# Kernel tuning notes

Hardware: AMD Instinct MI355X
Metric: run time of the kernel (lower is better)

Reference implementation:

```python
import jax, jax.numpy as jnp
import numpy as np

NUM_GRAPHS = 64
NUM_EDGE_TYPES = 3


def gat_conv(x, src, dst, W, a_src, a_dst, bias, num_nodes, heads, ch):
    # PyG GATConv, concat=False: mean over heads, attention leaky_relu slope 0.2
    xp = (x @ W).reshape(num_nodes, heads, ch)          # [N,H,C]
    al_s = jnp.einsum('nhc,hc->nh', xp, a_src)           # [N,H]
    al_d = jnp.einsum('nhc,hc->nh', xp, a_dst)
    logits = jax.nn.leaky_relu(al_s[src] + al_d[dst], 0.2)  # [E,H]
    m = jax.ops.segment_max(logits, dst, num_segments=num_nodes)
    e = jnp.exp(logits - m[dst])
    denom = jax.ops.segment_sum(e, dst, num_segments=num_nodes)
    alpha = e / denom[dst]                               # segment softmax over dst
    msg = alpha[:, :, None] * xp[src]                    # [E,H,C]
    out = jax.ops.segment_sum(msg, dst, num_segments=num_nodes)  # [N,H,C]
    return out.mean(axis=1) + bias


def lstm_dir(seq, w_ih, w_hh, b_ih, b_hh):
    # seq: [L,N,C]; PyTorch LSTM cell math
    hh = w_hh.shape[1]
    n = seq.shape[1]
    def step(carry, xt):
        h, c = carry
        g = xt @ w_ih.T + b_ih + h @ w_hh.T + b_hh
        i, f, gg, o = jnp.split(g, 4, axis=-1)
        c = jax.nn.sigmoid(f) * c + jax.nn.sigmoid(i) * jnp.tanh(gg)
        h = jax.nn.sigmoid(o) * jnp.tanh(c)
        return (h, c), h
    init = (jnp.zeros((n, hh), seq.dtype), jnp.zeros((n, hh), seq.dtype))
    _, hs = jax.lax.scan(step, init, seq)
    return hs  # [L,N,hh]


def setup_inputs() -> dict:
    key = jax.random.key(0)
    ks = jax.random.split(key, 24)
    N, E, C, H, P, T = 50000, 600000, 128, 4, 2, NUM_EDGE_TYPES
    HH = (P * C) // 2  # JK biLSTM hidden = 128
    s = 0.05
    src = jax.random.randint(ks[0], (E,), 0, N, dtype=jnp.int32)
    off = jax.random.randint(ks[1], (E,), 1, N, dtype=jnp.int32)
    dst = (src + off) % N  # guaranteed self-loop free
    edge_index = jnp.stack([src, dst], axis=0)  # types are contiguous blocks of E//T
    batch = jnp.sort(jax.random.randint(ks[2], (N,), 0, NUM_GRAPHS, dtype=jnp.int32))
    return {
        'x': jax.random.normal(ks[3], (N, C), jnp.float32),
        'edge_index': edge_index,
        'batch': batch,
        'problem_type': jax.random.uniform(ks[4], (NUM_GRAPHS, 1), jnp.float32),
        'gat_W': jax.random.normal(ks[5], (P, T, C, H * C), jnp.float32) * s,
        'gat_att_src': jax.random.normal(ks[6], (P, T, H, C), jnp.float32) * s,
        'gat_att_dst': jax.random.normal(ks[7], (P, T, H, C), jnp.float32) * s,
        'gat_bias': jnp.zeros((P, T, C), jnp.float32),
        'w_ih_fw': jax.random.normal(ks[8], (4 * HH, C), jnp.float32) * s,
        'w_hh_fw': jax.random.normal(ks[9], (4 * HH, HH), jnp.float32) * s,
        'b_ih_fw': jnp.zeros((4 * HH,), jnp.float32),
        'b_hh_fw': jnp.zeros((4 * HH,), jnp.float32),
        'w_ih_bw': jax.random.normal(ks[10], (4 * HH, C), jnp.float32) * s,
        'w_hh_bw': jax.random.normal(ks[11], (4 * HH, HH), jnp.float32) * s,
        'b_ih_bw': jnp.zeros((4 * HH,), jnp.float32),
        'b_hh_bw': jnp.zeros((4 * HH,), jnp.float32),
        'jk_att_w': jax.random.normal(ks[12], (2 * HH, 1), jnp.float32) * s,
        'jk_att_b': jnp.zeros((1,), jnp.float32),
        'fc1_w': jax.random.normal(ks[13], (C + 1, 80), jnp.float32) * s,
        'fc1_b': jnp.zeros((80,), jnp.float32),
        'fc2_w': jax.random.normal(ks[14], (80, 80), jnp.float32) * s,
        'fc2_b': jnp.zeros((80,), jnp.float32),
        'fc3_w': jax.random.normal(ks[15], (80, 10), jnp.float32) * s,
        'fc3_b': jnp.zeros((10,), jnp.float32),
    }


def reference(x, edge_index, batch, problem_type, gat_W, gat_att_src, gat_att_dst,
              gat_bias, w_ih_fw, w_hh_fw, b_ih_fw, b_hh_fw, w_ih_bw, w_hh_bw,
              b_ih_bw, b_hh_bw, jk_att_w, jk_att_b, fc1_w, fc1_b, fc2_w, fc2_b,
              fc3_w, fc3_b):
    N, C = x.shape
    P, T, H, _ = gat_att_src.shape
    E = edge_index.shape[1]
    Et = E // T  # edge types stored in contiguous blocks
    loop = jnp.arange(N, dtype=edge_index.dtype)
    xs = [x]
    cur = x
    for p in range(P):
        acc = jnp.zeros_like(cur)
        for t in range(T):
            src = jnp.concatenate([edge_index[0, t * Et:(t + 1) * Et], loop])
            dst = jnp.concatenate([edge_index[1, t * Et:(t + 1) * Et], loop])
            out = gat_conv(cur, src, dst, gat_W[p, t], gat_att_src[p, t],
                           gat_att_dst[p, t], gat_bias[p, t], N, H, C)
            acc = acc + jax.nn.leaky_relu(out)  # slope 0.01 (F.leaky_relu default)
        cur = acc / T
        xs.append(cur)
    seq = jnp.stack(xs, axis=0)  # [L,N,C], L=P+1
    hf = lstm_dir(seq, w_ih_fw, w_hh_fw, b_ih_fw, b_hh_fw)
    hb = lstm_dir(seq[::-1], w_ih_bw, w_hh_bw, b_ih_bw, b_hh_bw)[::-1]
    h = jnp.concatenate([hf, hb], axis=-1)  # [L,N,2*HH]
    score = jnp.einsum('lnh,ho->lno', h, jk_att_w)[..., 0] + jk_att_b[0]  # [L,N]
    alpha = jax.nn.softmax(score, axis=0)
    xjk = jnp.einsum('ln,lnc->nc', alpha, seq)  # JK-LSTM weighted sum
    pooled = jax.ops.segment_sum(xjk, batch, num_segments=NUM_GRAPHS)  # collate='sum'
    z = jnp.concatenate([pooled, problem_type], axis=1)
    z = jax.nn.leaky_relu(z @ fc1_w + fc1_b)
    z = jax.nn.leaky_relu(z @ fc2_w + fc2_b)
    return z @ fc3_w + fc3_b
```

## Files before the change

### kernel.cpp

```cpp
#include <hip/hip_runtime.h>
#include <cfloat>


typedef __attribute__((ext_vector_type(8))) short short8;
typedef __attribute__((ext_vector_type(4))) float f32x4;

#define DEG_CAP 31

__device__ __forceinline__ float lrelu(float x, float s) { return x > 0.f ? x : s * x; }

__device__ __forceinline__ float sigmf(float x) {
    return __builtin_amdgcn_rcpf(1.f + __expf(-x));
}
__device__ __forceinline__ float tanhf_fast(float x) {
    x = fminf(fmaxf(x, -15.f), 15.f);
    float e = __expf(2.f * x);
    return (e - 1.f) * __builtin_amdgcn_rcpf(e + 1.f);
}

__device__ __forceinline__ unsigned f2bf(float f) {
    unsigned u = __float_as_uint(f);
    return (u + 0x7FFFu + ((u >> 16) & 1u)) >> 16;
}
__device__ __forceinline__ float bf2f(ushort u) {
    return __uint_as_float(((unsigned)u) << 16);
}
__device__ __forceinline__ float bflo(unsigned u) {
    return __uint_as_float(u << 16);
}
__device__ __forceinline__ float bfhi(unsigned u) {
    return __uint_as_float(u & 0xFFFF0000u);
}

__device__ __forceinline__ int xcd_tile(int bid, int nwg) {
    int q = nwg >> 3, r = nwg & 7;
    int xcd = bid & 7, idx = bid >> 3;
    return (xcd < r ? xcd * (q + 1) : r * (q + 1) + (xcd - r) * q) + idx;
}

__device__ __forceinline__ void stage_a16(
    char* ldsA, const ushort* __restrict__ A, int row0, int M, int tid)
{
#pragma unroll
    for (int it = 0; it < 4; ++it) {
        int idx = it * 512 + tid;
        int r = idx >> 4, kc = (idx & 15) << 3;
        int row = row0 + r;
        uint4 v = make_uint4(0, 0, 0, 0);
        if (row < M) v = *(const uint4*)(A + (long)row * 128 + kc);
        *(uint4*)(ldsA + ((r * 256 + kc * 2) ^ ((r & 7) << 4))) = v;
    }
}
__device__ __forceinline__ void stage_b16(
    char* ldsB, const ushort* __restrict__ B, int tid)
{
#pragma unroll
    for (int it = 0; it < 4; ++it) {
        int idx = it * 512 + tid;
        int r = idx >> 4, kc = (idx & 15) << 3;
        *(uint4*)(ldsB + ((r * 256 + kc * 2) ^ ((r & 7) << 4))) =
            *(const uint4*)(B + (long)r * 128 + kc);
    }
}

__device__ __forceinline__ void compute_tile(
    const char* ldsA, const char* ldsB, f32x4 acc[2][4],
    int wr, int wc, int lr, int lk)
{
#pragma unroll
    for (int ks = 0; ks < 4; ++ks) {
        int kb = ks * 64 + lk;
        short8 af[2], bfr[4];
#pragma unroll
        for (int i = 0; i < 2; ++i) {
            int r = wr + i * 16 + lr;
            af[i] = *(const short8*)(ldsA + ((r * 256 + kb) ^ ((r & 7) << 4)));
        }
#pragma unroll
        for (int j = 0; j < 4; ++j) {
            int c = wc + j * 16 + lr;
            bfr[j] = *(const short8*)(ldsB + ((c * 256 + kb) ^ ((c & 7) << 4)));
        }
#pragma unroll
        for (int i = 0; i < 2; ++i)
#pragma unroll
            for (int j = 0; j < 4; ++j)
                acc[i][j] = __builtin_amdgcn_mfma_f32_16x16x32_bf16(af[i], bfr[j], acc[i][j], 0, 0, 0);
    }
}

__global__ __launch_bounds__(512, 4) void gemm_att(
    const ushort* __restrict__ A16, const ushort* __restrict__ Bt,
    ushort* __restrict__ C16, const float* __restrict__ a_s,
    const float* __restrict__ a_d, float* __restrict__ als,
    float* __restrict__ ald, int M, int nwg)
{
    __shared__ char lds[65536];
    __shared__ float smS[128], smD[128];
    char* ldsA = lds;
    char* ldsB = lds + 32768;
    const int tid = threadIdx.x;
    int tile = xcd_tile(blockIdx.x, nwg);
    int row0 = (tile >> 2) * 128;
    int h = tile & 3;
    int col0 = h * 128;
    if (tid < 128) { smS[tid] = 0.f; smD[tid] = 0.f; }
    stage_a16(ldsA, A16, row0, M, tid);
    stage_b16(ldsB, Bt + (long)col0 * 128, tid);
    __syncthreads();

    const int wv = tid >> 6, lane = tid & 63;
    const int wr = (wv & 3) * 32, wc = (wv >> 2) * 64;
    const int lr = lane & 15;
    const int lk = (lane >> 4) << 4;
    f32x4 acc[2][4] = {};
    compute_tile(ldsA, ldsB, acc, wr, wc, lr, lk);

    const float* asl = a_s + h * 128;
    const float* adl = a_d + h * 128;
#pragma unroll
    for (int i = 0; i < 2; ++i) {
#pragma unroll
        for (int q = 0; q < 4; ++q) {
            float ps = 0.f, pd = 0.f;
            int row = row0 + wr + i * 16 + (lane >> 4) * 4 + q;
#pragma unroll
            for (int j = 0; j < 4; ++j) {
                int cc = wc + j * 16 + lr;
                float v = acc[i][j][q];
                ps += v * asl[cc];
                pd += v * adl[cc];
                if (row < M) C16[(long)row * 512 + col0 + cc] = (ushort)f2bf(v);
            }
#pragma unroll
            for (int off = 8; off; off >>= 1) {
                ps += __shfl_xor(ps, off);
                pd += __shfl_xor(pd, off);
            }
            if (lr == 0) {
                int rl = wr + i * 16 + (lane >> 4) * 4 + q;
                atomicAdd(&smS[rl], ps);
                atomicAdd(&smD[rl], pd);
            }
        }
    }
    __syncthreads();
    if (tid < 128) {
        int row = row0 + tid;
        if (row < M) {
            als[(long)row * 4 + h] = smS[tid];
            ald[(long)row * 4 + h] = smD[tid];
        }
    }
}

__global__ __launch_bounds__(512, 4) void lstm_step(
    const ushort* __restrict__ Ab, const ushort* __restrict__ Bih,
    const ushort* __restrict__ Bhh, const ushort* __restrict__ hprev,
    ushort* __restrict__ hcur, ushort* __restrict__ cbuf,
    const float* __restrict__ bi, const float* __restrict__ bh,
    const float* __restrict__ jw, float* __restrict__ score,
    int N, int nwg, int first, int last)
{
    __shared__ char lds[65536];
    __shared__ float ssc[128];
    char* ldsA = lds;
    char* ldsB = lds + 32768;
    const int tid = threadIdx.x;
    int tile = xcd_tile(blockIdx.x, nwg);
    int row0 = (tile >> 2) * 128;
    int cc = tile & 3;
    if (tid < 128) ssc[tid] = 0.f;

    const int wv = tid >> 6, lane = tid & 63;
    const int wr = (wv & 3) * 32, wc = (wv >> 2) * 64;
    const int lr = lane & 15, lg = lane >> 4;
    const int lk = lg << 4;
    f32x4 acc[2][4] = {};

    stage_a16(ldsA, Ab, row0, N, tid);
    stage_b16(ldsB, Bih + (long)cc * 128 * 128, tid);
    __syncthreads();
    compute_tile(ldsA, ldsB, acc, wr, wc, lr, lk);
    if (!first) {
        __syncthreads();
        stage_a16(ldsA, hprev, row0, N, tid);
        stage_b16(ldsB, Bhh + (long)cc * 128 * 128, tid);
        __syncthreads();
        compute_tile(ldsA, ldsB, acc, wr, wc, lr, lk);
    }

    const int ch = cc * 32 + (wc >> 6) * 16 + lr;
    const float bI = bi[ch] + bh[ch];
    const float bF = bi[128 + ch] + bh[128 + ch];
    const float bG = bi[256 + ch] + bh[256 + ch];
    const float bO = bi[384 + ch] + bh[384 + ch];
    const float jv = jw[ch];
    float psum[8];
#pragma unroll
    for (int i = 0; i < 2; ++i) {
#pragma unroll
        for (int q = 0; q < 4; ++q) {
            int u = i * 4 + q;
            int row = row0 + wr + i * 16 + lg * 4 + q;
            float p = 0.f;
            if (row < N) {
                long off = (long)row * 128 + ch;
                float cprev = first ? 0.f : bf2f(cbuf[off]);
                float cv = sigmf(acc[i][1][q] + bF) * cprev
                         + sigmf(acc[i][0][q] + bI) * tanhf_fast(acc[i][2][q] + bG);
                float hv = sigmf(acc[i][3][q] + bO) * tanhf_fast(cv);
                if (!last) {
                    cbuf[off] = (ushort)f2bf(cv);
                    hcur[off] = (ushort)f2bf(hv);
                }
                p = hv * jv;
            }
            psum[u] = p;
        }
    }
#pragma unroll
    for (int u = 0; u < 8; ++u) {
        float p = psum[u];
#pragma unroll
        for (int off = 8; off; off >>= 1) p += __shfl_xor(p, off);
        if (lr == 0)
            atomicAdd(&ssc[wr + (u >> 2) * 16 + lg * 4 + (u & 3)], p);
    }
    __syncthreads();
    if (tid < 128) {
        int row = row0 + tid;
        if (row < N) unsafeAtomicAdd(&score[row], ssc[tid]);
    }
}

__global__ void pack_gatw(const float* __restrict__ gw, ushort* __restrict__ out) {
    int i = blockIdx.x * 256 + threadIdx.x;
    if (i >= 6 * 65536) return;
    int pt = i >> 16, rem = i & 65535, n = rem >> 7, k = rem & 127;
    out[i] = (ushort)f2bf(gw[pt * 65536 + k * 512 + n]);
}
__global__ void pack_lstm(const float* __restrict__ a, const float* __restrict__ b,
                          const float* __restrict__ c, const float* __restrict__ d,
                          ushort* __restrict__ out) {
    int i = blockIdx.x * 256 + threadIdx.x;
    if (i >= 4 * 65536) return;
    const float* p = (i < 65536) ? a : (i < 131072) ? b : (i < 196608) ? c : d;
    int rem = i & 65535;
    int cp = rem >> 7, k = rem & 127;
    int g = (cp >> 4) & 3;
    int ch = ((cp >> 6) << 4) | (cp & 15);
    out[i] = (ushort)f2bf(p[(g * 128 + ch) * 128 + k]);
}
__global__ void pack_x(const float* __restrict__ x, ushort* __restrict__ o, long n) {
    long i = ((long)blockIdx.x * 256 + threadIdx.x) * 4;
    if (i >= n) return;
    float4 v = *(const float4*)(x + i);
    ushort4 u;
    u.x = (ushort)f2bf(v.x); u.y = (ushort)f2bf(v.y);
    u.z = (ushort)f2bf(v.z); u.w = (ushort)f2bf(v.w);
    *(ushort4*)(o + i) = u;
}

__global__ __launch_bounds__(256) void build_csr(
    const int* __restrict__ srcs, const int* __restrict__ dsts,
    int E, int Et, int N, int* __restrict__ cnt, int* __restrict__ bucket)
{
    int i = blockIdx.x * 256 + threadIdx.x;
    if (i >= E) return;
    int t = i / Et;
    int s = srcs[i];
    int d = dsts[i];
    int slot = atomicAdd(&cnt[t * N + d], 1);
    if (slot < DEG_CAP) bucket[((long)(t * N + d)) * DEG_CAP + slot] = s;
}

__global__ __launch_bounds__(256) void gat_gather(
    const int* __restrict__ cnt, const int* __restrict__ bucket,
    const float* __restrict__ als, const float* __restrict__ ald,
    const ushort* __restrict__ xp16, const float* __restrict__ bias,
    float* __restrict__ dstb, ushort* __restrict__ out16, int N, int t, int first)
{
    int lane = threadIdx.x & 63;
    int half = lane >> 5, hl = lane & 31;
    int d = blockIdx.x * 8 + (threadIdx.x >> 6) * 2 + half;
    if (d >= N) d = N - 1;
    int deg = min(cnt[t * N + d], DEG_CAP);
    int s = d;
    if (hl < deg) s = bucket[((long)(t * N + d)) * DEG_CAP + hl];
    bool act = (hl <= deg);
    float4 ad = *(const float4*)(ald + (long)d * 4);
    float l0 = -FLT_MAX, l1 = -FLT_MAX, l2 = -FLT_MAX, l3 = -FLT_MAX;
    if (act) {
        float4 as = *(const float4*)(als + (long)s * 4);
        l0 = lrelu(as.x + ad.x, 0.2f);
        l1 = lrelu(as.y + ad.y, 0.2f);
        l2 = lrelu(as.z + ad.z, 0.2f);
        l3 = lrelu(as.w + ad.w, 0.2f);
    }
    float m0 = l0, m1 = l1, m2 = l2, m3 = l3;
#pragma unroll
    for (int off = 16; off; off >>= 1) {
        m0 = fmaxf(m0, __shfl_xor(m0, off));
        m1 = fmaxf(m1, __shfl_xor(m1, off));
        m2 = fmaxf(m2, __shfl_xor(m2, off));
        m3 = fmaxf(m3, __shfl_xor(m3, off));
    }
    float e0 = 0.f, e1 = 0.f, e2 = 0.f, e3 = 0.f;
    if (act) {
        e0 = __expf(l0 - m0); e1 = __expf(l1 - m1);
        e2 = __expf(l2 - m2); e3 = __expf(l3 - m3);
    }
    float s0 = e0, s1 = e1, s2 = e2, s3 = e3;
#pragma unroll
    for (int off = 16; off; off >>= 1) {
        s0 += __shfl_xor(s0, off);
        s1 += __shfl_xor(s1, off);
        s2 += __shfl_xor(s2, off);
        s3 += __shfl_xor(s3, off);
    }
    float a0 = 0.25f * e0 / s0, a1 = 0.25f * e1 / s1;
    float a2 = 0.25f * e2 / s2, a3 = 0.25f * e3 / s3;

    int md = deg;
#pragma unroll
    for (int off = 32; off; off >>= 1) md = max(md, __shfl_xor(md, off));

    int base = (lane & 32);
    float accL[2] = {0.f, 0.f}, accH[2] = {0.f, 0.f};
    int sj = __shfl(s, base);
    const uint* xs = (const uint*)(xp16 + (long)sj * 512);
    uint c0 = xs[hl], c1 = xs[32 + hl], c2 = xs[64 + hl], c3 = xs[96 + hl];
    uint c4 = xs[128 + hl], c5 = xs[160 + hl], c6 = xs[192 + hl], c7 = xs[224 + hl];
    for (int j = 0; j < md; ++j) {
        int sn = __shfl(s, base + j + 1);
        const uint* xn = (const uint*)(xp16 + (long)sn * 512);
        uint n0 = xn[hl], n1 = xn[32 + hl], n2 = xn[64 + hl], n3 = xn[96 + hl];
        uint n4 = xn[128 + hl], n5 = xn[160 + hl], n6 = xn[192 + hl], n7 = xn[224 + hl];
        float w0 = __shfl(a0, base + j), w1 = __shfl(a1, base + j);
        float w2 = __shfl(a2, base + j), w3 = __shfl(a3, base + j);
        accL[0] += w0 * bflo(c0) + w1 * bflo(c2) + w2 * bflo(c4) + w3 * bflo(c6);
        accH[0] += w0 * bfhi(c0) + w1 * bfhi(c2) + w2 * bfhi(c4) + w3 * bfhi(c6);
        accL[1] += w0 * bflo(c1) + w1 * bflo(c3) + w2 * bflo(c5) + w3 * bflo(c7);
        accH[1] += w0 * bfhi(c1) + w1 * bfhi(c3) + w2 * bfhi(c5) + w3 * bfhi(c7);
        c0 = n0; c1 = n1; c2 = n2; c3 = n3;
        c4 = n4; c5 = n5; c6 = n6; c7 = n7;
    }
    {
        float w0 = __shfl(a0, base + md), w1 = __shfl(a1, base + md);
        float w2 = __shfl(a2, base + md), w3 = __shfl(a3, base + md);
        accL[0] += w0 * bflo(c0) + w1 * bflo(c2) + w2 * bflo(c4) + w3 * bflo(c6);
        accH[0] += w0 * bfhi(c0) + w1 * bfhi(c2) + w2 * bfhi(c4) + w3 * bfhi(c6);
        accL[1] += w0 * bflo(c1) + w1 * bflo(c3) + w2 * bflo(c5) + w3 * bflo(c7);
        accH[1] += w0 * bfhi(c1) + w1 * bfhi(c3) + w2 * bfhi(c5) + w3 * bfhi(c7);
    }

    int chA = 2 * hl;
    int chB = 64 + 2 * hl;
    float r0 = lrelu(accL[0] + bias[chA], 0.01f) * (1.f / 3.f);
    float r1 = lrelu(accH[0] + bias[chA + 1], 0.01f) * (1.f / 3.f);
    float r2 = lrelu(accL[1] + bias[chB], 0.01f) * (1.f / 3.f);
    float r3 = lrelu(accH[1] + bias[chB + 1], 0.01f) * (1.f / 3.f);
    float2* apA = (float2*)(dstb + (long)d * 128) + hl;
    float2* apB = (float2*)(dstb + (long)d * 128 + 64) + hl;
    float2 fA, fB;
    if (first) { fA.x = r0; fA.y = r1; fB.x = r2; fB.y = r3; }
    else {
        float2 pA = *apA, pB = *apB;
        fA.x = pA.x + r0; fA.y = pA.y + r1;
        fB.x = pB.x + r2; fB.y = pB.y + r3;
    }
    *apA = fA; *apB = fB;
    if (out16) {
        ushort2 uA, uB;
        uA.x = (ushort)f2bf(fA.x); uA.y = (ushort)f2bf(fA.y);
        uB.x = (ushort)f2bf(fB.x); uB.y = (ushort)f2bf(fB.y);
        *((ushort2*)(out16 + (long)d * 128) + hl) = uA;
        *((ushort2*)(out16 + (long)d * 128 + 64) + hl) = uB;
    }
}

__global__ void init_z0(const float* __restrict__ ptype, float* __restrict__ z0) {
    int i = blockIdx.x * 128 + threadIdx.x;
    if (i < 64 * 129) z0[i] = ((i % 129) == 128) ? ptype[i / 129] : 0.f;
}

__global__ __launch_bounds__(128) void pool_jk(
    const float* __restrict__ score, const float* __restrict__ x0,
    const float* __restrict__ x1, const float* __restrict__ x2,
    const int* __restrict__ batch, float* __restrict__ z0, int N)
{
    int c = threadIdx.x;
    int n0 = blockIdx.x * 64;
    if (n0 >= N) return;
    int n1 = min(n0 + 64, N);
    float s = 0.f;
    int g = batch[n0];
    for (int n = n0; n < n1; ++n) {
        int b = batch[n];
        if (b != g) { unsafeAtomicAdd(&z0[g * 129 + c], s); s = 0.f; g = b; }
        float s0 = score[n], s1 = score[N + n], s2 = score[2L * N + n];
        float m = fmaxf(s0, fmaxf(s1, s2));
        float e0 = __expf(s0 - m), e1 = __expf(s1 - m), e2 = __expf(s2 - m);
        float inv = __builtin_amdgcn_rcpf(e0 + e1 + e2);
        long i = (long)n * 128 + c;
        s += (e0 * x0[i] + e1 * x1[i] + e2 * x2[i]) * inv;
    }
    unsafeAtomicAdd(&z0[g * 129 + c], s);
}

__global__ __launch_bounds__(128) void mlp_kernel(
    const float* __restrict__ z0, const float* __restrict__ w1, const float* __restrict__ b1,
    const float* __restrict__ w2, const float* __restrict__ b2,
    const float* __restrict__ w3, const float* __restrict__ b3,
    float* __restrict__ out)
{
    int gidx = blockIdx.x, tid = threadIdx.x;
    __shared__ float zin[129], z1[80], z2[80];
    zin[tid] = z0[gidx * 129 + tid];
    if (tid == 0) zin[128] = z0[gidx * 129 + 128];
    __syncthreads();
    if (tid < 80) {
        float s = b1[tid];
        for (int k = 0; k < 129; ++k) s += zin[k] * w1[k * 80 + tid];
        z1[tid] = lrelu(s, 0.01f);
    }
    __syncthreads();
    if (tid < 80) {
        float s = b2[tid];
        for (int k = 0; k < 80; ++k) s += z1[k] * w2[k * 80 + tid];
        z2[tid] = lrelu(s, 0.01f);
    }
    __syncthreads();
    if (tid < 10) {
        float s = b3[tid];
        for (int k = 0; k < 80; ++k) s += z2[k] * w3[k * 10 + tid];
        out[gidx * 10 + tid] = s;
    }
}

extern "C" void kernel_launch(void* const* d_in, const int* in_sizes, int n_in,
                              void* d_out, int out_size, void* d_ws, size_t ws_size,
                              hipStream_t stream)
{
    (void)n_in; (void)out_size; (void)ws_size;
    const float* x      = (const float*)d_in[0];
    const int*   ei     = (const int*)d_in[1];
    const int*   batch  = (const int*)d_in[2];
    const float* ptype  = (const float*)d_in[3];
    const float* gatW   = (const float*)d_in[4];
    const float* gatAs  = (const float*)d_in[5];
    const float* gatAd  = (const float*)d_in[6];
    const float* gatB   = (const float*)d_in[7];
    const float* w_ih_fw = (const float*)d_in[8];
    const float* w_hh_fw = (const float*)d_in[9];
    const float* b_ih_fw = (const float*)d_in[10];
    const float* b_hh_fw = (const float*)d_in[11];
    const float* w_ih_bw = (const float*)d_in[12];
    const float* w_hh_bw = (const float*)d_in[13];
    const float* b_ih_bw = (const float*)d_in[14];
    const float* b_hh_bw = (const float*)d_in[15];
    const float* jkw    = (const float*)d_in[16];
    const float* fc1w   = (const float*)d_in[18];
    const float* fc1b   = (const float*)d_in[19];
    const float* fc2w   = (const float*)d_in[20];
    const float* fc2b   = (const float*)d_in[21];
    const float* fc3w   = (const float*)d_in[22];
    const float* fc3b   = (const float*)d_in[23];

    const int N = in_sizes[0] / 128;
    const int E = in_sizes[1] / 2;
    const int Et = E / 3;
    const long NC = (long)N * 128;

    float* w = (float*)d_ws;
    float* xp   = w; w += (long)N * 512;
    float* l1   = w; w += NC;
    float* l2   = w; w += NC;
    float* accb = w; w += NC;
    float* outm = w; w += NC;
    ushort* xb16 = (ushort*)w; w += 3L * N * 64;
    float* als  = w; w += (long)N * 4;
    float* ald  = w; w += (long)N * 4;
    float* score = w; w += 3L * N;
    ushort* gwt = (ushort*)w; w += 6 * 65536 / 2;
    ushort* lwt = (ushort*)w; w += 4 * 65536 / 2;
    float* z0   = w; w += 64 * 129 + 4;

    int* cnt    = (int*)outm;
    int* bucket = cnt + 3L * N;
    ushort* xp16 = (ushort*)xp;
    ushort* h0 = xp16 + (long)N * 512;
    ushort* h1 = h0 + NC;

    pack_gatw<<<(6 * 65536 + 255) / 256, 256, 0, stream>>>(gatW, gwt);
    pack_lstm<<<(4 * 65536 + 255) / 256, 256, 0, stream>>>(w_ih_fw, w_hh_fw, w_ih_bw, w_hh_bw, lwt);
    pack_x<<<(int)((NC / 4 + 255) / 256), 256, 0, stream>>>(x, xb16, NC);
    hipMemsetAsync(score, 0, sizeof(float) * 3 * N, stream);
    hipMemsetAsync(cnt, 0, sizeof(int) * 3 * N, stream);
    build_csr<<<(E + 255) / 256, 256, 0, stream>>>(ei, ei + E, E, Et, N, cnt, bucket);

    const int RB = (N + 127) / 128;
    const int nwg = RB * 4;

    for (int p = 0; p < 2; ++p) {
        const ushort* curA = xb16 + (long)p * N * 128;
        float* dstb = (p == 0) ? l1 : l2;
        ushort* d16 = xb16 + (long)(p + 1) * N * 128;
        for (int t = 0; t < 3; ++t) {
            int pt = p * 3 + t;
            gemm_att<<<nwg, 512, 0, stream>>>(curA, gwt + (long)pt * 65536, xp16,
                                              gatAs + pt * 512, gatAd + pt * 512,
                                              als, ald, N, nwg);
            gat_gather<<<(N + 7) / 8, 256, 0, stream>>>(cnt, bucket, als, ald, xp16,
                                                        gatB + pt * 128, dstb,
                                                        (t == 2) ? d16 : nullptr,
                                                        N, t, t == 0);
        }
    }

    ushort* cbuf = (ushort*)outm;
    for (int dir = 0; dir < 2; ++dir) {
        const ushort* Bih = lwt + (long)(dir ? 2 : 0) * 65536;
        const ushort* Bhh = lwt + (long)(dir ? 3 : 1) * 65536;
        const float* bi = dir ? b_ih_bw : b_ih_fw;
        const float* bh = dir ? b_hh_bw : b_hh_fw;
        const float* jw = jkw + (dir ? 128 : 0);
        ushort* hp = h0;
        ushort* hc = h1;
        for (int j = 0; j < 3; ++j) {
            int l = dir ? (2 - j) : j;
            const ushort* Ab = xb16 + (long)l * N * 128;
            lstm_step<<<nwg, 512, 0, stream>>>(Ab, Bih, Bhh, hp, hc, cbuf,
                                               bi, bh, jw, score + (long)l * N,
                                               N, nwg, j == 0, j == 2);
            ushort* tmp = hp; hp = hc; hc = tmp;
        }
    }

    init_z0<<<65, 128, 0, stream>>>(ptype, z0);
    pool_jk<<<(N + 63) / 64, 128, 0, stream>>>(score, x, l1, l2, batch, z0, N);
    mlp_kernel<<<64, 128, 0, stream>>>(z0, fc1w, fc1b, fc2w, fc2b, fc3w, fc3b,
                                       (float*)d_out);
}
```

Baseline: 778.2 us.

## Stage GEMM tiles via global_load_lds and fuse both LSTM directions per launch

Tile staging now uses direct global-to-LDS loads with the XOR swizzle applied on the source address, replacing the loads through registers followed by LDS stores. Out-of-range rows are clamped to the last row instead of zero-filled. The forward and backward LSTM passes now run in one launch per timestep using a 2D grid, so six launches become three and each grid is twice as large. Each direction gets its own h and c buffers, which uses more workspace.

```diff
diff --git a/kernel.cpp b/kernel.cpp
--- a/kernel.cpp
+++ b/kernel.cpp
@@ -38,28 +38,39 @@
     return (xcd < r ? xcd * (q + 1) : r * (q + 1) + (xcd - r) * q) + idx;
 }
 
-__device__ __forceinline__ void stage_a16(
+__device__ __forceinline__ void stage_a_glds(
     char* ldsA, const ushort* __restrict__ A, int row0, int M, int tid)
 {
+    int wv = tid >> 6, lane = tid & 63;
 #pragma unroll
     for (int it = 0; it < 4; ++it) {
-        int idx = it * 512 + tid;
-        int r = idx >> 4, kc = (idx & 15) << 3;
-        int row = row0 + r;
-        uint4 v = make_uint4(0, 0, 0, 0);
-        if (row < M) v = *(const uint4*)(A + (long)row * 128 + kc);
-        *(uint4*)(ldsA + ((r * 256 + kc * 2) ^ ((r & 7) << 4))) = v;
-    }
-}
-__device__ __forceinline__ void stage_b16(
+        int chunk = it * 8 + wv;
+        int d = chunk * 1024 + lane * 16;
+        int r = d >> 8;
+        int col = (d & 255) ^ ((r & 7) << 4);
+        int row = min(row0 + r, M - 1);
+        const char* src = (const char*)A + (long)row * 256 + col;
+        __builtin_amdgcn_global_load_lds(
+            (const __attribute__((address_space(1))) void*)src,
+            (__attribute__((address_space(3))) void*)(ldsA + chunk * 1024),
+            16, 0, 0);
+    }
+}
+__device__ __forceinline__ void stage_b_glds(
     char* ldsB, const ushort* __restrict__ B, int tid)
 {
+    int wv = tid >> 6, lane = tid & 63;
 #pragma unroll
     for (int it = 0; it < 4; ++it) {
-        int idx = it * 512 + tid;
-        int r = idx >> 4, kc = (idx & 15) << 3;
-        *(uint4*)(ldsB + ((r * 256 + kc * 2) ^ ((r & 7) << 4))) =
-            *(const uint4*)(B + (long)r * 128 + kc);
+        int chunk = it * 8 + wv;
+        int d = chunk * 1024 + lane * 16;
+        int r = d >> 8;
+        int col = (d & 255) ^ ((r & 7) << 4);
+        const char* src = (const char*)B + (long)r * 256 + col;
+        __builtin_amdgcn_global_load_lds(
+            (const __attribute__((address_space(1))) void*)src,
+            (__attribute__((address_space(3))) void*)(ldsB + chunk * 1024),
+            16, 0, 0);
     }
 }
 
@@ -105,8 +116,8 @@
     int h = tile & 3;
     int col0 = h * 128;
     if (tid < 128) { smS[tid] = 0.f; smD[tid] = 0.f; }
-    stage_a16(ldsA, A16, row0, M, tid);
-    stage_b16(ldsB, Bt + (long)col0 * 128, tid);
+    stage_a_glds(ldsA, A16, row0, M, tid);
+    stage_b_glds(ldsB, Bt + (long)col0 * 128, tid);
     __syncthreads();
 
     const int wv = tid >> 6, lane = tid & 63;
@@ -154,23 +165,37 @@
     }
 }
 
-__global__ __launch_bounds__(512, 4) void lstm_step(
-    const ushort* __restrict__ Ab, const ushort* __restrict__ Bih,
-    const ushort* __restrict__ Bhh, const ushort* __restrict__ hprev,
-    ushort* __restrict__ hcur, ushort* __restrict__ cbuf,
-    const float* __restrict__ bi, const float* __restrict__ bh,
-    const float* __restrict__ jw, float* __restrict__ score,
-    int N, int nwg, int first, int last)
+__global__ __launch_bounds__(512, 4) void lstm_both(
+    const ushort* __restrict__ xb, const ushort* __restrict__ lwt,
+    ushort* __restrict__ hbase, ushort* __restrict__ cbase,
+    const float* __restrict__ bihf, const float* __restrict__ bhhf,
+    const float* __restrict__ bihb, const float* __restrict__ bhhb,
+    const float* __restrict__ jkw, float* __restrict__ score,
+    int N, int nwg, int jstep)
 {
     __shared__ char lds[65536];
     __shared__ float ssc[128];
     char* ldsA = lds;
     char* ldsB = lds + 32768;
     const int tid = threadIdx.x;
+    const int dir = blockIdx.y;
     int tile = xcd_tile(blockIdx.x, nwg);
     int row0 = (tile >> 2) * 128;
     int cc = tile & 3;
     if (tid < 128) ssc[tid] = 0.f;
+
+    const int l = dir ? (2 - jstep) : jstep;
+    const int first = (jstep == 0), last = (jstep == 2);
+    const ushort* Ab = xb + (long)l * N * 128;
+    const ushort* Bih = lwt + (long)dir * 2 * 65536;
+    const ushort* Bhh = Bih + 65536;
+    const ushort* hprev = hbase + (long)((dir << 1) | ((jstep + 1) & 1)) * N * 128;
+    ushort* hcur = hbase + (long)((dir << 1) | (jstep & 1)) * N * 128;
+    ushort* cbuf = cbase + (long)dir * N * 128;
+    const float* bi = dir ? bihb : bihf;
+    const float* bh = dir ? bhhb : bhhf;
+    const float* jw = jkw + (dir ? 128 : 0);
+    float* sc = score + (long)l * N;
 
     const int wv = tid >> 6, lane = tid & 63;
     const int wr = (wv & 3) * 32, wc = (wv >> 2) * 64;
@@ -178,14 +203,14 @@
     const int lk = lg << 4;
     f32x4 acc[2][4] = {};
 
-    stage_a16(ldsA, Ab, row0, N, tid);
-    stage_b16(ldsB, Bih + (long)cc * 128 * 128, tid);
+    stage_a_glds(ldsA, Ab, row0, N, tid);
+    stage_b_glds(ldsB, Bih + (long)cc * 128 * 128, tid);
     __syncthreads();
     compute_tile(ldsA, ldsB, acc, wr, wc, lr, lk);
     if (!first) {
         __syncthreads();
-        stage_a16(ldsA, hprev, row0, N, tid);
-        stage_b16(ldsB, Bhh + (long)cc * 128 * 128, tid);
+        stage_a_glds(ldsA, hprev, row0, N, tid);
+        stage_b_glds(ldsB, Bhh + (long)cc * 128 * 128, tid);
         __syncthreads();
         compute_tile(ldsA, ldsB, acc, wr, wc, lr, lk);
     }
@@ -230,7 +255,7 @@
     __syncthreads();
     if (tid < 128) {
         int row = row0 + tid;
-        if (row < N) unsafeAtomicAdd(&score[row], ssc[tid]);
+        if (row < N) unsafeAtomicAdd(&sc[row], ssc[tid]);
     }
 }
 
@@ -490,8 +515,8 @@
     int* cnt    = (int*)outm;
     int* bucket = cnt + 3L * N;
     ushort* xp16 = (ushort*)xp;
-    ushort* h0 = xp16 + (long)N * 512;
-    ushort* h1 = h0 + NC;
+    ushort* hbase = xp16 + (long)N * 512;
+    ushort* cbase = (ushort*)outm;
 
     pack_gatw<<<(6 * 65536 + 255) / 256, 256, 0, stream>>>(gatW, gwt);
     pack_lstm<<<(4 * 65536 + 255) / 256, 256, 0, stream>>>(w_ih_fw, w_hh_fw, w_ih_bw, w_hh_bw, lwt);
@@ -519,23 +544,10 @@
         }
     }
 
-    ushort* cbuf = (ushort*)outm;
-    for (int dir = 0; dir < 2; ++dir) {
-        const ushort* Bih = lwt + (long)(dir ? 2 : 0) * 65536;
-        const ushort* Bhh = lwt + (long)(dir ? 3 : 1) * 65536;
-        const float* bi = dir ? b_ih_bw : b_ih_fw;
-        const float* bh = dir ? b_hh_bw : b_hh_fw;
-        const float* jw = jkw + (dir ? 128 : 0);
-        ushort* hp = h0;
-        ushort* hc = h1;
-        for (int j = 0; j < 3; ++j) {
-            int l = dir ? (2 - j) : j;
-            const ushort* Ab = xb16 + (long)l * N * 128;
-            lstm_step<<<nwg, 512, 0, stream>>>(Ab, Bih, Bhh, hp, hc, cbuf,
-                                               bi, bh, jw, score + (long)l * N,
-                                               N, nwg, j == 0, j == 2);
-            ushort* tmp = hp; hp = hc; hc = tmp;
-        }
+    for (int j = 0; j < 3; ++j) {
+        lstm_both<<<dim3(nwg, 2), 512, 0, stream>>>(
+            xb16, lwt, hbase, cbase, b_ih_fw, b_hh_fw, b_ih_bw, b_hh_bw,
+            jkw, score, N, nwg, j);
     }
 
     init_z0<<<65, 128, 0, stream>>>(ptype, z0);
```

Result: faster. 723.5 us (-7.0%).
